# Optimization experiments

Measured on AMD Instinct MI355X. Metric: run time of the kernel, lower is better.

The kernel has to match this reference:

```python
import jax, jax.numpy as jnp
from jax import lax
import numpy as np

B, T, N, C_IN = 32, 24, 2048, 2
HID, EMB, HORIZON, OUT_DIM = 64, 16, 12, 1


def setup_inputs() -> dict:
    key = jax.random.key(0)
    ks = jax.random.split(key, 8)
    s = 0.05
    return {
        "x": jax.random.normal(ks[0], (B, T, N, C_IN), dtype=jnp.float32),
        "E": jax.random.normal(ks[1], (N, EMB), dtype=jnp.float32),
        "W1": jax.random.normal(ks[2], (C_IN + HID, 4 * HID), dtype=jnp.float32) * s,
        "b1": jnp.zeros((4 * HID,), dtype=jnp.float32),
        "W2": jax.random.normal(ks[3], (HID + HID, 4 * HID), dtype=jnp.float32) * s,
        "b2": jnp.zeros((4 * HID,), dtype=jnp.float32),
        "Wp": jax.random.normal(ks[4], (HID, OUT_DIM * HORIZON), dtype=jnp.float32) * s,
        "bp": jnp.zeros((OUT_DIM * HORIZON,), dtype=jnp.float32),
    }


def _cell(A, xt, h, c, W, b):
    # Graph-conv LSTM cell: A @ [x, h] -> 4 gates
    comb = jnp.concatenate([xt, h], axis=-1)            # [B,N,in+H]
    conv = jnp.einsum("nm,bmc->bnc", A, comb)           # adaptive graph conv
    gates = conv @ W + b                                  # [B,N,4H]
    i, f, g, o = jnp.split(gates, 4, axis=-1)
    c_new = jax.nn.sigmoid(f) * c + jax.nn.sigmoid(i) * jnp.tanh(g)
    h_new = jax.nn.sigmoid(o) * jnp.tanh(c_new)
    return h_new, c_new


def reference(x, E, W1, b1, W2, b2, Wp, bp):
    # Adaptive adjacency: softmax(relu(E E^T)) row-normalized
    A = jax.nn.softmax(jax.nn.relu(E @ E.T), axis=1)      # [N,N]
    b, t, n, _ = x.shape
    z = jnp.zeros((b, n, HID), dtype=x.dtype)
    init = ((z, z), (z, z))

    def step(carry, xt):
        (h1, c1), (h2, c2) = carry
        h1, c1 = _cell(A, xt, h1, c1, W1, b1)
        h2, c2 = _cell(A, h1, h2, c2, W2, b2)
        return ((h1, c1), (h2, c2)), None

    carry, _ = lax.scan(step, init, jnp.moveaxis(x, 1, 0))  # scan over T
    h_last = carry[1][0]                                     # [B,N,H]
    out = h_last @ Wp + bp                                   # [B,N,HORIZON*OUT]
    out = out.reshape(b, n, HORIZON, OUT_DIM).transpose(0, 2, 1, 3)
    return out                                               # [B,HORIZON,N,OUT]
```

## Files before the change

### kernel.cpp

```cpp
#include <hip/hip_runtime.h>
#include <hip/hip_bf16.h>
#include <cstddef>
#include <cstdint>

#define NN   2048
#define BB   32
#define TT   24
#define CIN  2
#define HH   64
#define EMBD 16
#define HOR  12
#define XC   (TT*BB*CIN)
#define PW   4096
#define KC   6144
#define NT   96

using bfrag  = __attribute__((ext_vector_type(8))) short;
using f32x4  = __attribute__((ext_vector_type(4))) float;

static __device__ __forceinline__ short f2bf(float f) {
    __hip_bfloat16 h = __float2bfloat16(f);
    return *reinterpret_cast<short*>(&h);
}
static __device__ __forceinline__ float bf2f(short s) {
    __hip_bfloat16 h;
    *reinterpret_cast<short*>(&h) = s;
    return __bfloat162float(h);
}
static __device__ __forceinline__ unsigned int packsplit(float v) {
    short hb = f2bf(v);
    short lb = f2bf(v - bf2f(hb));
    return (unsigned int)(unsigned short)hb | ((unsigned int)(unsigned short)lb << 16);
}
static __device__ __forceinline__ float fsig(float x) {
    return __builtin_amdgcn_rcpf(1.f + __expf(-x));
}
static __device__ __forceinline__ float ftanh(float x) {
    return 1.f - 2.f*__builtin_amdgcn_rcpf(1.f + __expf(2.f*x));
}

#define AS1 __attribute__((address_space(1)))
#define AS3 __attribute__((address_space(3)))
static __device__ __forceinline__ void gload16(const short* g, short* l) {
    __builtin_amdgcn_global_load_lds((const AS1 void*)g, (AS3 void*)l, 16, 0, 0);
}

__global__ __launch_bounds__(256) void compute_A_kernel(const float* __restrict__ E,
                                                        short* __restrict__ A2) {
    __shared__ float srow[NN];
    __shared__ float sred[256];
    int row = blockIdx.x;
    float er[EMBD];
#pragma unroll
    for (int k = 0; k < EMBD; ++k) er[k] = E[row*EMBD + k];
    float lmax = -1e30f;
    for (int j = threadIdx.x; j < NN; j += 256) {
        const float* ej = E + j*EMBD;
        float d = 0.f;
#pragma unroll
        for (int k = 0; k < EMBD; ++k) d = fmaf(er[k], ej[k], d);
        d = fmaxf(d, 0.f);
        srow[j] = d;
        lmax = fmaxf(lmax, d);
    }
    sred[threadIdx.x] = lmax;
    __syncthreads();
    for (int s = 128; s > 0; s >>= 1) {
        if (threadIdx.x < s) sred[threadIdx.x] = fmaxf(sred[threadIdx.x], sred[threadIdx.x+s]);
        __syncthreads();
    }
    float rmax = sred[0];
    __syncthreads();
    float lsum = 0.f;
    for (int j = threadIdx.x; j < NN; j += 256) {
        float e = expf(srow[j] - rmax);
        srow[j] = e;
        lsum += e;
    }
    sred[threadIdx.x] = lsum;
    __syncthreads();
    for (int s = 128; s > 0; s >>= 1) {
        if (threadIdx.x < s) sred[threadIdx.x] += sred[threadIdx.x+s];
        __syncthreads();
    }
    float rinv = 1.f / sred[0];
    for (int j = threadIdx.x; j < NN; j += 256) {
        float v = srow[j] * rinv;
        short h = f2bf(v);
        short l = f2bf(v - bf2f(h));
        size_t base = (size_t)row*KC + j;
        A2[base]        = h;
        A2[base + 2048] = h;
        A2[base + 4096] = l;
    }
}

__global__ void scatter_xall(const float* __restrict__ x,
                             short* __restrict__ hi, short* __restrict__ lo) {
    int idx = blockIdx.x*256 + threadIdx.x;
    int n = idx & (NN-1);
    int col = idx >> 11;
    int c = col & 1, b = (col >> 1) & 31, t = col >> 6;
    float v = x[(size_t)(((size_t)b*TT + t)*NN + n)*CIN + c];
    short h = f2bf(v);
    size_t o = (size_t)col*NN + n;
    hi[o] = h;
    lo[o] = f2bf(v - bf2f(h));
}

__global__ void wsplit_T(const float* __restrict__ W, int rowoff, int Kd,
                         short* __restrict__ hi, short* __restrict__ lo) {
    int id = blockIdx.x*256 + threadIdx.x;
    if (id >= 256*Kd) return;
    int j = id / Kd, c = id - j*Kd;
    float v = W[(size_t)(rowoff + c)*256 + j];
    short h = f2bf(v);
    hi[id] = h;
    lo[id] = f2bf(v - bf2f(h));
}

__global__ __launch_bounds__(256, 3) void gc3_gemm(
        const short* __restrict__ Ahi, const short* __restrict__ Alo,
        const short* __restrict__ Bhi, const short* __restrict__ Blo,
        float* __restrict__ Cout, int outStride, int astr) {
    __shared__ short As[12288];
    short* AsHi = As;
    short* AsLo = As + 2048;
    short* BsHi = As + 4096;
    short* BsLo = As + 8192;
    const int t = threadIdx.x;
    const int w = t >> 6, lane = t & 63;
    const int wm = w >> 1, wn = w & 1;
    const int fr = lane & 15, fc = lane >> 4;
    const int rowbase = blockIdx.y * 64;
    const int colbase = blockIdx.x * 128;

    const int rp = t >> 3, ql = t & 7;
    const int qs = ql ^ (rp & 7);
    const int srow = rp*2 + (qs >> 2);
    const int sch  = (qs & 3) * 8;
    const short* aHiS = Ahi + (size_t)(rowbase + srow)*astr + sch;
    const short* aLoS = Alo + (size_t)(rowbase + srow)*astr + sch;
    const short* bHiS = Bhi + (size_t)(colbase + srow)*NN + sch;
    const short* bLoS = Blo + (size_t)(colbase + srow)*NN + sch;
    const size_t bHalf = (size_t)64*NN;

    short* aHiD  = AsHi + t*8;
    short* aLoD  = AsLo + t*8;
    short* bHiD0 = BsHi + t*8;
    short* bHiD1 = BsHi + 2048 + t*8;
    short* bLoD0 = BsLo + t*8;
    short* bLoD1 = BsLo + 2048 + t*8;

    auto ldsoff = [](int row, int f) {
        int rr = row >> 1;
        int q = (((row & 1) << 2) | f) ^ (rr & 7);
        return rr*64 + q*8;
    };
    int aoff[2], boff[4];
#pragma unroll
    for (int m = 0; m < 2; ++m) aoff[m] = ldsoff(wm*32 + m*16 + fr, fc);
#pragma unroll
    for (int n = 0; n < 4; ++n) boff[n] = ldsoff(wn*64 + n*16 + fr, fc);

    f32x4 acc[2][4];
#pragma unroll
    for (int m = 0; m < 2; ++m)
#pragma unroll
        for (int n = 0; n < 4; ++n)
#pragma unroll
            for (int r = 0; r < 4; ++r) acc[m][n][r] = 0.f;

    for (int k0 = 0; k0 < NN; k0 += 32) {
        gload16(aHiS, aHiD);
        gload16(aLoS, aLoD);
        gload16(bHiS, bHiD0);
        gload16(bHiS + bHalf, bHiD1);
        gload16(bLoS, bLoD0);
        gload16(bLoS + bHalf, bLoD1);
        aHiS += 32; aLoS += 32; bHiS += 32; bLoS += 32;
        __syncthreads();
        bfrag ah[2], al[2], bh[4], bl[4];
#pragma unroll
        for (int m = 0; m < 2; ++m) {
            ah[m] = *(const bfrag*)(AsHi + aoff[m]);
            al[m] = *(const bfrag*)(AsLo + aoff[m]);
        }
#pragma unroll
        for (int n = 0; n < 4; ++n) {
            bh[n] = *(const bfrag*)(BsHi + boff[n]);
            bl[n] = *(const bfrag*)(BsLo + boff[n]);
        }
#pragma unroll
        for (int m = 0; m < 2; ++m)
#pragma unroll
            for (int n = 0; n < 4; ++n) {
                acc[m][n] = __builtin_amdgcn_mfma_f32_16x16x32_bf16(ah[m], bh[n], acc[m][n], 0, 0, 0);
                acc[m][n] = __builtin_amdgcn_mfma_f32_16x16x32_bf16(ah[m], bl[n], acc[m][n], 0, 0, 0);
                acc[m][n] = __builtin_amdgcn_mfma_f32_16x16x32_bf16(al[m], bh[n], acc[m][n], 0, 0, 0);
            }
        __syncthreads();
    }
#pragma unroll
    for (int m = 0; m < 2; ++m) {
        const int gr = rowbase + wm*32 + m*16 + fc*4;
#pragma unroll
        for (int n = 0; n < 4; ++n) {
            const int gc = colbase + wn*64 + n*16 + fr;
#pragma unroll
            for (int r = 0; r < 4; ++r)
                Cout[(size_t)(gr + r)*outStride + gc] = acc[m][n][r];
        }
    }
}

__global__ __launch_bounds__(512, 2) void gemm8p(
        const short* __restrict__ A2, const short* __restrict__ B2,
        unsigned int* __restrict__ Cpk, int colstart) {
    __shared__ short lds[3*24576];
    const int tid = threadIdx.x;
    const int w = tid >> 6, lane = tid & 63;
    const int wm = w >> 2, wn = w & 3;
    const int fr = lane & 15, fc = lane >> 4;
    const int gx = gridDim.x;
    const int nwg = gx * gridDim.y;
    const int fid = blockIdx.y * gx + blockIdx.x;
    const int swz = (fid & 7) * (nwg >> 3) + (fid >> 3);
    const int rowbase = (swz / gx) * 128;
    const int colbase = colstart + (swz % gx) * 256;

    const int srl = tid >> 3;
    const int sck = (tid & 7) ^ (srl & 7);
    const short* aS0 = A2 + (size_t)(rowbase + srl)*KC + sck*8;
    const short* aS1 = A2 + (size_t)(rowbase + 64 + srl)*KC + sck*8;
    const short* bS0 = B2 + (size_t)(colbase + srl)*KC + sck*8;
    const short* bS1 = B2 + (size_t)(colbase + 64 + srl)*KC + sck*8;
    const short* bS2 = B2 + (size_t)(colbase + 128 + srl)*KC + sck*8;
    const short* bS3 = B2 + (size_t)(colbase + 192 + srl)*KC + sck*8;

    auto sw = [](int row, int chunk) {
        int c2 = chunk ^ (row & 7);
        return row*64 + c2*8;
    };
    int aoff[4][2], boff[4][2];
#pragma unroll
    for (int m = 0; m < 4; ++m)
#pragma unroll
        for (int kk = 0; kk < 2; ++kk)
            aoff[m][kk] = sw(wm*64 + m*16 + fr, kk*4 + fc);
#pragma unroll
    for (int n = 0; n < 4; ++n)
#pragma unroll
        for (int kk = 0; kk < 2; ++kk)
            boff[n][kk] = 8192 + sw(wn*64 + n*16 + fr, kk*4 + fc);

    bfrag a[4], b[4];
    f32x4 acc[4][4];
#pragma unroll
    for (int m = 0; m < 4; ++m)
#pragma unroll
        for (int n = 0; n < 4; ++n)
#pragma unroll
            for (int r = 0; r < 4; ++r) acc[m][n][r] = 0.f;

    short* bC = lds;
    short* bN = lds + 24576;
    short* bP = lds + 49152;

    gload16(aS0, bC + tid*8);            gload16(aS1, bC + 4096 + tid*8);
    gload16(bS0, bC + 8192 + tid*8);     gload16(bS1, bC + 12288 + tid*8);
    gload16(bS2, bC + 16384 + tid*8);    gload16(bS3, bC + 20480 + tid*8);
    gload16(aS0 + 64, bN + tid*8);          gload16(aS1 + 64, bN + 4096 + tid*8);
    gload16(bS0 + 64, bN + 8192 + tid*8);   gload16(bS1 + 64, bN + 12288 + tid*8);
    gload16(bS2 + 64, bN + 16384 + tid*8);  gload16(bS3 + 64, bN + 20480 + tid*8);

    for (int t = 0; t < NT; ++t) {
        if (t < NT-1) { asm volatile("s_waitcnt vmcnt(6)" ::: "memory"); }
        else          { asm volatile("s_waitcnt vmcnt(0)" ::: "memory"); }
        __builtin_amdgcn_s_barrier();
        if (t + 2 < NT) {
            const int toff = (t + 2) * 64;
            gload16(aS0 + toff, bP + tid*8);
            gload16(aS1 + toff, bP + 4096 + tid*8);
            gload16(bS0 + toff, bP + 8192 + tid*8);
            gload16(bS1 + toff, bP + 12288 + tid*8);
            gload16(bS2 + toff, bP + 16384 + tid*8);
            gload16(bS3 + toff, bP + 20480 + tid*8);
        }
        __builtin_amdgcn_sched_barrier(0);
#pragma unroll
        for (int kk = 0; kk < 2; ++kk) {
#pragma unroll
            for (int m = 0; m < 4; ++m) a[m] = *(const bfrag*)(bC + aoff[m][kk]);
#pragma unroll
            for (int n = 0; n < 4; ++n) b[n] = *(const bfrag*)(bC + boff[n][kk]);
            __builtin_amdgcn_sched_barrier(0);
            __builtin_amdgcn_s_setprio(1);
#pragma unroll
            for (int m = 0; m < 4; ++m)
#pragma unroll
                for (int n = 0; n < 4; ++n)
                    acc[m][n] = __builtin_amdgcn_mfma_f32_16x16x32_bf16(
                        a[m], b[n], acc[m][n], 0, 0, 0);
            __builtin_amdgcn_s_setprio(0);
            __builtin_amdgcn_sched_barrier(0);
        }
        short* tmp = bC; bC = bN; bN = bP; bP = tmp;
    }
#pragma unroll
    for (int m = 0; m < 4; ++m) {
        const int gr0 = rowbase + wm*64 + m*16 + fc*4;
#pragma unroll
        for (int n = 0; n < 4; ++n) {
            const int gc = colbase + wn*64 + n*16 + fr;
#pragma unroll
            for (int r = 0; r < 4; ++r)
                Cpk[(size_t)(gr0 + r)*PW + gc] = packsplit(acc[m][n][r]);
        }
    }
}

template<int NCH, bool XEP>
static __device__ __forceinline__ void cell_body(
        const unsigned int* __restrict__ P,
        const float* __restrict__ convX,
        const float* __restrict__ Wx,
        const short* __restrict__ Wthi, const short* __restrict__ Wtlo,
        const float* __restrict__ bias,
        float* __restrict__ cbuf,
        short* __restrict__ hout,
        int tstep, int n0blk, int b) {
    const int t = threadIdx.x;
    const int w = t >> 6, lane = t & 63;
    const int fr = lane & 15, fc = lane >> 4;
    constexpr int KW = NCH*32;

    bfrag bh[4][NCH], bl[4][NCH];
#pragma unroll
    for (int g = 0; g < 4; ++g)
#pragma unroll
        for (int ch = 0; ch < NCH; ++ch) {
            size_t o = (size_t)((g*4 + w)*16 + fr)*KW + ch*32 + fc*8;
            bh[g][ch] = *(const bfrag*)(Wthi + o);
            bl[g][ch] = *(const bfrag*)(Wtlo + o);
        }
    const int k = w*16 + fr;
    float bs[4], wx0[4], wx1[4];
#pragma unroll
    for (int g = 0; g < 4; ++g) {
        bs[g] = bias[g*64 + k];
        if (XEP) { wx0[g] = Wx[g*64 + k]; wx1[g] = Wx[256 + g*64 + k]; }
    }
    int colb[NCH];
#pragma unroll
    for (int ch = 0; ch < NCH; ++ch)
        colb[ch] = (NCH == 2 || ch < 2) ? (2048 + b*64 + ch*32)
                                        : (b*64 + (ch-2)*32);
    const int cc = lane >> 4;
    const size_t crow = (size_t)(b*64 + k)*NN;
    const size_t hrow = (size_t)(b*64 + k)*KC;

    for (int nt = 0; nt < 8; ++nt) {
        const int n0 = n0blk + nt*16;
        bfrag ah[NCH], al[NCH];
#pragma unroll
        for (int ch = 0; ch < NCH; ++ch) {
            const unsigned int* ap = P + (size_t)(n0 + fr)*PW + colb[ch] + fc*8;
            uint4 u0 = *(const uint4*)ap;
            uint4 u1 = *(const uint4*)(ap + 4);
            unsigned int uu[8] = {u0.x,u0.y,u0.z,u0.w,u1.x,u1.y,u1.z,u1.w};
#pragma unroll
            for (int i = 0; i < 8; ++i) {
                ah[ch][i] = (short)(uu[i] & 0xffffu);
                al[ch][i] = (short)(uu[i] >> 16);
            }
        }
        f32x4 acc[4];
#pragma unroll
        for (int g = 0; g < 4; ++g)
#pragma unroll
            for (int r = 0; r < 4; ++r) acc[g][r] = 0.f;
#pragma unroll
        for (int ch = 0; ch < NCH; ++ch)
#pragma unroll
            for (int g = 0; g < 4; ++g) {
                acc[g] = __builtin_amdgcn_mfma_f32_16x16x32_bf16(ah[ch], bh[g][ch], acc[g], 0, 0, 0);
                acc[g] = __builtin_amdgcn_mfma_f32_16x16x32_bf16(ah[ch], bl[g][ch], acc[g], 0, 0, 0);
                acc[g] = __builtin_amdgcn_mfma_f32_16x16x32_bf16(al[ch], bh[g][ch], acc[g], 0, 0, 0);
            }
        const int nb = n0 + cc*4;
        float4 cold = *(const float4*)(cbuf + crow + nb);
        float xa0[4], xa1[4];
        if (XEP) {
#pragma unroll
            for (int r = 0; r < 4; ++r) {
                float2 cx = *(const float2*)(convX + (size_t)(nb + r)*XC + tstep*64 + b*2);
                xa0[r] = cx.x; xa1[r] = cx.y;
            }
        }
        float cn[4], hv[4];
#pragma unroll
        for (int r = 0; r < 4; ++r) {
            float pg[4];
#pragma unroll
            for (int g = 0; g < 4; ++g) {
                pg[g] = acc[g][r] + bs[g];
                if (XEP) pg[g] += xa0[r]*wx0[g] + xa1[r]*wx1[g];
            }
            float gi = fsig(pg[0]);
            float gf = fsig(pg[1]);
            float gg = ftanh(pg[2]);
            float go = fsig(pg[3]);
            float co = (&cold.x)[r];
            cn[r] = gf*co + gi*gg;
            hv[r] = go * ftanh(cn[r]);
        }
        *(float4*)(cbuf + crow + nb) = make_float4(cn[0], cn[1], cn[2], cn[3]);
        short hh[4], hl[4];
#pragma unroll
        for (int r = 0; r < 4; ++r) {
            hh[r] = f2bf(hv[r]);
            hl[r] = f2bf(hv[r] - bf2f(hh[r]));
        }
        short4 h4 = make_short4(hh[0], hh[1], hh[2], hh[3]);
        short4 l4 = make_short4(hl[0], hl[1], hl[2], hl[3]);
        *(short4*)(hout + hrow + nb)        = h4;
        *(short4*)(hout + hrow + 2048 + nb) = l4;
        *(short4*)(hout + hrow + 4096 + nb) = h4;
    }
}

template<int NCH, bool XEP>
__global__ __launch_bounds__(256, 2) void cell_mfma(
        const unsigned int* __restrict__ P,
        const float* __restrict__ convX,
        const float* __restrict__ Wx,
        const short* __restrict__ Wthi, const short* __restrict__ Wtlo,
        const float* __restrict__ bias,
        float* __restrict__ cbuf,
        short* __restrict__ hout,
        int tstep) {
    cell_body<NCH, XEP>(P, convX, Wx, Wthi, Wtlo, bias, cbuf, hout,
                        tstep, blockIdx.x*128, blockIdx.y);
}

__global__ __launch_bounds__(256, 2) void cell_fused(
        const unsigned int* __restrict__ P,
        const float* __restrict__ convX,
        const float* __restrict__ Wx1,
        const short* __restrict__ Wt2hi, const short* __restrict__ Wt2lo,
        const short* __restrict__ Wt1hi, const short* __restrict__ Wt1lo,
        const float* __restrict__ b2v, const float* __restrict__ b1v,
        float* __restrict__ cs2, float* __restrict__ cs1,
        short* __restrict__ h2out, short* __restrict__ h1out,
        int tnext) {
    if (blockIdx.z == 0)
        cell_body<4, false>(P, nullptr, nullptr, Wt2hi, Wt2lo, b2v, cs2, h2out,
                            0, blockIdx.x*128, blockIdx.y);
    else
        cell_body<2, true>(P, convX, Wx1, Wt1hi, Wt1lo, b1v, cs1, h1out,
                           tnext, blockIdx.x*128, blockIdx.y);
}

__global__ __launch_bounds__(256) void proj_T(const short* __restrict__ B2,
        const float* __restrict__ Wp, const float* __restrict__ bp,
        float* __restrict__ out) {
    __shared__ float sW[HH*HOR];
    __shared__ float sb[HOR];
    for (int i = threadIdx.x; i < HH*HOR; i += 256) sW[i] = Wp[i];
    if (threadIdx.x < HOR) sb[threadIdx.x] = bp[threadIdx.x];
    __syncthreads();
    int idx = blockIdx.x*256 + threadIdx.x;
    int b = idx >> 11, n = idx & (NN-1);
    float acc[HOR];
#pragma unroll
    for (int j = 0; j < HOR; ++j) acc[j] = sb[j];
    for (int k = 0; k < HH; ++k) {
        size_t row = (size_t)(b*64 + k)*KC + n;
        float h = bf2f(B2[row]) + bf2f(B2[row + 2048]);
#pragma unroll
        for (int j = 0; j < HOR; ++j) acc[j] = fmaf(h, sW[k*HOR + j], acc[j]);
    }
#pragma unroll
    for (int j = 0; j < HOR; ++j)
        out[(size_t)(b*HOR + j)*NN + n] = acc[j];
}

extern "C" void kernel_launch(void* const* d_in, const int* in_sizes, int n_in,
                              void* d_out, int out_size, void* d_ws, size_t ws_size,
                              hipStream_t stream) {
    const float* x  = (const float*)d_in[0];
    const float* E  = (const float*)d_in[1];
    const float* W1 = (const float*)d_in[2];
    const float* b1 = (const float*)d_in[3];
    const float* W2 = (const float*)d_in[4];
    const float* b2 = (const float*)d_in[5];
    const float* Wp = (const float*)d_in[6];
    const float* bp = (const float*)d_in[7];
    float* out = (float*)d_out;

    char* base = (char*)d_ws;
    short* A2     = (short*)base; base += (size_t)NN*KC*2;
    float* convX  = (float*)base; base += (size_t)NN*XC*4;
    unsigned int* P = (unsigned int*)base; base += (size_t)NN*PW*4;
    short* B2     = (short*)base; base += (size_t)PW*KC*2;
    float* cs1    = (float*)base; base += (size_t)NN*NN*4;
    float* cs2    = (float*)base; base += (size_t)NN*NN*4;
    short* Wt2hi  = (short*)base; base += 256*128*2;
    short* Wt2lo  = (short*)base; base += 256*128*2;
    short* Wt1hi  = (short*)base; base += 256*64*2;
    short* Wt1lo  = (short*)base; base += 256*64*2;
    short* XThi = (short*)P;
    short* XTlo = XThi + (size_t)XC*NN;
    short* h2out = B2;
    short* h1out = B2 + (size_t)NN*KC;

    hipMemsetAsync(cs1, 0, (size_t)NN*NN*4, stream);
    hipMemsetAsync(cs2, 0, (size_t)NN*NN*4, stream);

    compute_A_kernel<<<NN, 256, 0, stream>>>(E, A2);
    wsplit_T<<<(256*128 + 255)/256, 256, 0, stream>>>(W2, 0, 128, Wt2hi, Wt2lo);
    wsplit_T<<<(256*64 + 255)/256, 256, 0, stream>>>(W1, 2, 64, Wt1hi, Wt1lo);
    scatter_xall<<<(XC*NN)/256, 256, 0, stream>>>(x, XThi, XTlo);
    gc3_gemm<<<dim3(XC/128, NN/64), 256, 0, stream>>>(
        A2, A2 + 4096, XThi, XTlo, convX, XC, KC);
    hipMemsetAsync(P, 0, (size_t)NN*PW*4, stream);

    cell_mfma<2, true><<<dim3(NN/128, BB), 256, 0, stream>>>(
        P, convX, W1, Wt1hi, Wt1lo, b1, cs1, h1out, 0);
    gemm8p<<<dim3(8, 16), 512, 0, stream>>>(A2, B2, P, 2048);

    for (int t = 0; t < TT; ++t) {
        if (t < TT-1) {
            cell_fused<<<dim3(NN/128, BB, 2), 256, 0, stream>>>(
                P, convX, W1, Wt2hi, Wt2lo, Wt1hi, Wt1lo, b2, b1,
                cs2, cs1, h2out, h1out, t+1);
            gemm8p<<<dim3(16, 16), 512, 0, stream>>>(A2, B2, P, 0);
        } else {
            cell_mfma<4, false><<<dim3(NN/128, BB), 256, 0, stream>>>(
                P, nullptr, nullptr, Wt2hi, Wt2lo, b2, cs2, h2out, 0);
        }
    }
    proj_T<<<(BB*NN)/256, 256, 0, stream>>>(B2, Wp, bp, out);
}
```

Measured before the change: 3.768 ms.

## Store bf16 hi/lo splits separately and issue three 32x32 MFMAs per tile

Replaces the concatenated [hi,hi,lo]×[hi,lo,hi] K=6144 layout with separate hi and lo arrays of K=2048. The per-step graph-conv GEMM now loads each hi fragment once and issues three 32x32x16 MFMAs (hi·hi, hi·lo, lo·hi). This cuts duplicated global and LDS traffic for the hi parts, and the 32x32 MFMA shape is meant to raise MFMA throughput. The cell kernels, the A builder and the projection are updated to write and read the split buffers, and the epilogue maps the 16-value accumulator layout.

```diff
diff --git a/kernel.cpp b/kernel.cpp
--- a/kernel.cpp
+++ b/kernel.cpp
@@ -12,11 +12,12 @@
 #define HOR  12
 #define XC   (TT*BB*CIN)
 #define PW   4096
-#define KC   6144
-#define NT   96
+#define NT2  64
+#define HOFF ((size_t)2048*NN)
 
 using bfrag  = __attribute__((ext_vector_type(8))) short;
 using f32x4  = __attribute__((ext_vector_type(4))) float;
+using f32x16 = __attribute__((ext_vector_type(16))) float;
 
 static __device__ __forceinline__ short f2bf(float f) {
     __hip_bfloat16 h = __float2bfloat16(f);
@@ -46,7 +47,8 @@
 }
 
 __global__ __launch_bounds__(256) void compute_A_kernel(const float* __restrict__ E,
-                                                        short* __restrict__ A2) {
+                                                        short* __restrict__ Ahi,
+                                                        short* __restrict__ Alo) {
     __shared__ float srow[NN];
     __shared__ float sred[256];
     int row = blockIdx.x;
@@ -87,11 +89,8 @@
     for (int j = threadIdx.x; j < NN; j += 256) {
         float v = srow[j] * rinv;
         short h = f2bf(v);
-        short l = f2bf(v - bf2f(h));
-        size_t base = (size_t)row*KC + j;
-        A2[base]        = h;
-        A2[base + 2048] = h;
-        A2[base + 4096] = l;
+        Ahi[(size_t)row*NN + j] = h;
+        Alo[(size_t)row*NN + j] = f2bf(v - bf2f(h));
     }
 }
 
@@ -122,7 +121,7 @@
 __global__ __launch_bounds__(256, 3) void gc3_gemm(
         const short* __restrict__ Ahi, const short* __restrict__ Alo,
         const short* __restrict__ Bhi, const short* __restrict__ Blo,
-        float* __restrict__ Cout, int outStride, int astr) {
+        float* __restrict__ Cout, int outStride) {
     __shared__ short As[12288];
     short* AsHi = As;
     short* AsLo = As + 2048;
@@ -139,8 +138,8 @@
     const int qs = ql ^ (rp & 7);
     const int srow = rp*2 + (qs >> 2);
     const int sch  = (qs & 3) * 8;
-    const short* aHiS = Ahi + (size_t)(rowbase + srow)*astr + sch;
-    const short* aLoS = Alo + (size_t)(rowbase + srow)*astr + sch;
+    const short* aHiS = Ahi + (size_t)(rowbase + srow)*NN + sch;
+    const short* aLoS = Alo + (size_t)(rowbase + srow)*NN + sch;
     const short* bHiS = Bhi + (size_t)(colbase + srow)*NN + sch;
     const short* bLoS = Blo + (size_t)(colbase + srow)*NN + sch;
     const size_t bHalf = (size_t)64*NN;
@@ -214,14 +213,15 @@
     }
 }
 
-__global__ __launch_bounds__(512, 2) void gemm8p(
-        const short* __restrict__ A2, const short* __restrict__ B2,
+__global__ __launch_bounds__(512, 2) void gcsplit(
+        const short* __restrict__ Ahi, const short* __restrict__ Alo,
+        const short* __restrict__ Bhi, const short* __restrict__ Blo,
         unsigned int* __restrict__ Cpk, int colstart) {
     __shared__ short lds[3*24576];
     const int tid = threadIdx.x;
     const int w = tid >> 6, lane = tid & 63;
     const int wm = w >> 2, wn = w & 3;
-    const int fr = lane & 15, fc = lane >> 4;
+    const int lr = lane & 31, lh = lane >> 5;
     const int gx = gridDim.x;
     const int nwg = gx * gridDim.y;
     const int fid = blockIdx.y * gx + blockIdx.x;
@@ -229,93 +229,98 @@
     const int rowbase = (swz / gx) * 128;
     const int colbase = colstart + (swz % gx) * 256;
 
-    const int srl = tid >> 3;
-    const int sck = (tid & 7) ^ (srl & 7);
-    const short* aS0 = A2 + (size_t)(rowbase + srl)*KC + sck*8;
-    const short* aS1 = A2 + (size_t)(rowbase + 64 + srl)*KC + sck*8;
-    const short* bS0 = B2 + (size_t)(colbase + srl)*KC + sck*8;
-    const short* bS1 = B2 + (size_t)(colbase + 64 + srl)*KC + sck*8;
-    const short* bS2 = B2 + (size_t)(colbase + 128 + srl)*KC + sck*8;
-    const short* bS3 = B2 + (size_t)(colbase + 192 + srl)*KC + sck*8;
-
-    auto sw = [](int row, int chunk) {
-        int c2 = chunk ^ (row & 7);
-        return row*64 + c2*8;
+    const int srow = tid >> 2;
+    const int sc   = (tid & 3) ^ ((srow >> 1) & 3);
+    const short* aHiS  = Ahi + (size_t)(rowbase + srow)*NN + sc*8;
+    const short* aLoS  = Alo + (size_t)(rowbase + srow)*NN + sc*8;
+    const short* bHiS0 = Bhi + (size_t)(colbase + srow)*NN + sc*8;
+    const short* bHiS1 = Bhi + (size_t)(colbase + 128 + srow)*NN + sc*8;
+    const short* bLoS0 = Blo + (size_t)(colbase + srow)*NN + sc*8;
+    const short* bLoS1 = Blo + (size_t)(colbase + 128 + srow)*NN + sc*8;
+
+    auto sw2 = [](int row, int c) {
+        return row*32 + (c ^ ((row >> 1) & 3))*8;
     };
-    int aoff[4][2], boff[4][2];
-#pragma unroll
-    for (int m = 0; m < 4; ++m)
-#pragma unroll
-        for (int kk = 0; kk < 2; ++kk)
-            aoff[m][kk] = sw(wm*64 + m*16 + fr, kk*4 + fc);
-#pragma unroll
-    for (int n = 0; n < 4; ++n)
-#pragma unroll
-        for (int kk = 0; kk < 2; ++kk)
-            boff[n][kk] = 8192 + sw(wn*64 + n*16 + fr, kk*4 + fc);
-
-    bfrag a[4], b[4];
-    f32x4 acc[4][4];
-#pragma unroll
-    for (int m = 0; m < 4; ++m)
-#pragma unroll
-        for (int n = 0; n < 4; ++n)
-#pragma unroll
-            for (int r = 0; r < 4; ++r) acc[m][n][r] = 0.f;
+    int aoffH[2][2], boffH[2][2];
+#pragma unroll
+    for (int m = 0; m < 2; ++m)
+#pragma unroll
+        for (int ks = 0; ks < 2; ++ks)
+            aoffH[m][ks] = sw2(wm*64 + m*32 + lr, ks*2 + lh);
+#pragma unroll
+    for (int n = 0; n < 2; ++n)
+#pragma unroll
+        for (int ks = 0; ks < 2; ++ks)
+            boffH[n][ks] = 8192 + sw2(wn*64 + n*32 + lr, ks*2 + lh);
+
+    f32x16 acc[2][2];
+#pragma unroll
+    for (int m = 0; m < 2; ++m)
+#pragma unroll
+        for (int n = 0; n < 2; ++n)
+#pragma unroll
+            for (int r = 0; r < 16; ++r) acc[m][n][r] = 0.f;
 
     short* bC = lds;
     short* bN = lds + 24576;
     short* bP = lds + 49152;
 
-    gload16(aS0, bC + tid*8);            gload16(aS1, bC + 4096 + tid*8);
-    gload16(bS0, bC + 8192 + tid*8);     gload16(bS1, bC + 12288 + tid*8);
-    gload16(bS2, bC + 16384 + tid*8);    gload16(bS3, bC + 20480 + tid*8);
-    gload16(aS0 + 64, bN + tid*8);          gload16(aS1 + 64, bN + 4096 + tid*8);
-    gload16(bS0 + 64, bN + 8192 + tid*8);   gload16(bS1 + 64, bN + 12288 + tid*8);
-    gload16(bS2 + 64, bN + 16384 + tid*8);  gload16(bS3 + 64, bN + 20480 + tid*8);
-
-    for (int t = 0; t < NT; ++t) {
-        if (t < NT-1) { asm volatile("s_waitcnt vmcnt(6)" ::: "memory"); }
-        else          { asm volatile("s_waitcnt vmcnt(0)" ::: "memory"); }
+    auto STAGE = [&](short* dst, int koff) {
+        gload16(aHiS  + koff, dst + tid*8);
+        gload16(aLoS  + koff, dst + 4096  + tid*8);
+        gload16(bHiS0 + koff, dst + 8192  + tid*8);
+        gload16(bHiS1 + koff, dst + 12288 + tid*8);
+        gload16(bLoS0 + koff, dst + 16384 + tid*8);
+        gload16(bLoS1 + koff, dst + 20480 + tid*8);
+    };
+    STAGE(bC, 0);
+    STAGE(bN, 32);
+
+    for (int t = 0; t < NT2; ++t) {
+        if (t < NT2-1) { asm volatile("s_waitcnt vmcnt(6)" ::: "memory"); }
+        else           { asm volatile("s_waitcnt vmcnt(0)" ::: "memory"); }
         __builtin_amdgcn_s_barrier();
-        if (t + 2 < NT) {
-            const int toff = (t + 2) * 64;
-            gload16(aS0 + toff, bP + tid*8);
-            gload16(aS1 + toff, bP + 4096 + tid*8);
-            gload16(bS0 + toff, bP + 8192 + tid*8);
-            gload16(bS1 + toff, bP + 12288 + tid*8);
-            gload16(bS2 + toff, bP + 16384 + tid*8);
-            gload16(bS3 + toff, bP + 20480 + tid*8);
-        }
+        if (t + 2 < NT2) STAGE(bP, (t + 2) * 32);
         __builtin_amdgcn_sched_barrier(0);
 #pragma unroll
-        for (int kk = 0; kk < 2; ++kk) {
-#pragma unroll
-            for (int m = 0; m < 4; ++m) a[m] = *(const bfrag*)(bC + aoff[m][kk]);
-#pragma unroll
-            for (int n = 0; n < 4; ++n) b[n] = *(const bfrag*)(bC + boff[n][kk]);
+        for (int ks = 0; ks < 2; ++ks) {
+            bfrag ah[2], al[2], bh[2], bl[2];
+#pragma unroll
+            for (int m = 0; m < 2; ++m) {
+                ah[m] = *(const bfrag*)(bC + aoffH[m][ks]);
+                al[m] = *(const bfrag*)(bC + 4096 + aoffH[m][ks]);
+            }
+#pragma unroll
+            for (int n = 0; n < 2; ++n) {
+                bh[n] = *(const bfrag*)(bC + boffH[n][ks]);
+                bl[n] = *(const bfrag*)(bC + 8192 + boffH[n][ks]);
+            }
             __builtin_amdgcn_sched_barrier(0);
             __builtin_amdgcn_s_setprio(1);
 #pragma unroll
-            for (int m = 0; m < 4; ++m)
-#pragma unroll
-                for (int n = 0; n < 4; ++n)
-                    acc[m][n] = __builtin_amdgcn_mfma_f32_16x16x32_bf16(
-                        a[m], b[n], acc[m][n], 0, 0, 0);
+            for (int m = 0; m < 2; ++m)
+#pragma unroll
+                for (int n = 0; n < 2; ++n) {
+                    acc[m][n] = __builtin_amdgcn_mfma_f32_32x32x16_bf16(ah[m], bh[n], acc[m][n], 0, 0, 0);
+                    acc[m][n] = __builtin_amdgcn_mfma_f32_32x32x16_bf16(ah[m], bl[n], acc[m][n], 0, 0, 0);
+                    acc[m][n] = __builtin_amdgcn_mfma_f32_32x32x16_bf16(al[m], bh[n], acc[m][n], 0, 0, 0);
+                }
             __builtin_amdgcn_s_setprio(0);
             __builtin_amdgcn_sched_barrier(0);
         }
         short* tmp = bC; bC = bN; bN = bP; bP = tmp;
     }
 #pragma unroll
-    for (int m = 0; m < 4; ++m) {
-        const int gr0 = rowbase + wm*64 + m*16 + fc*4;
-#pragma unroll
-        for (int n = 0; n < 4; ++n) {
-            const int gc = colbase + wn*64 + n*16 + fr;
-#pragma unroll
-            for (int r = 0; r < 4; ++r)
-                Cpk[(size_t)(gr0 + r)*PW + gc] = packsplit(acc[m][n][r]);
+    for (int m = 0; m < 2; ++m) {
+        const int gr0 = rowbase + wm*64 + m*32 + 4*lh;
+#pragma unroll
+        for (int n = 0; n < 2; ++n) {
+            const int gc = colbase + wn*64 + n*32 + lr;
+#pragma unroll
+            for (int r = 0; r < 16; ++r) {
+                int gr = gr0 + (r & 3) + 8*(r >> 2);
+                Cpk[(size_t)gr*PW + gc] = packsplit(acc[m][n][r]);
+            }
         }
     }
 }
@@ -328,21 +333,21 @@
         const short* __restrict__ Wthi, const short* __restrict__ Wtlo,
         const float* __restrict__ bias,
         float* __restrict__ cbuf,
-        short* __restrict__ hout,
+        short* __restrict__ bhi, short* __restrict__ blo,
         int tstep, int n0blk, int b) {
     const int t = threadIdx.x;
     const int w = t >> 6, lane = t & 63;
     const int fr = lane & 15, fc = lane >> 4;
     constexpr int KW = NCH*32;
 
-    bfrag bh[4][NCH], bl[4][NCH];
+    bfrag bhw[4][NCH], blw[4][NCH];
 #pragma unroll
     for (int g = 0; g < 4; ++g)
 #pragma unroll
         for (int ch = 0; ch < NCH; ++ch) {
             size_t o = (size_t)((g*4 + w)*16 + fr)*KW + ch*32 + fc*8;
-            bh[g][ch] = *(const bfrag*)(Wthi + o);
-            bl[g][ch] = *(const bfrag*)(Wtlo + o);
+            bhw[g][ch] = *(const bfrag*)(Wthi + o);
+            blw[g][ch] = *(const bfrag*)(Wtlo + o);
         }
     const int k = w*16 + fr;
     float bs[4], wx0[4], wx1[4];
@@ -358,7 +363,6 @@
                                         : (b*64 + (ch-2)*32);
     const int cc = lane >> 4;
     const size_t crow = (size_t)(b*64 + k)*NN;
-    const size_t hrow = (size_t)(b*64 + k)*KC;
 
     for (int nt = 0; nt < 8; ++nt) {
         const int n0 = n0blk + nt*16;
@@ -384,9 +388,9 @@
         for (int ch = 0; ch < NCH; ++ch)
 #pragma unroll
             for (int g = 0; g < 4; ++g) {
-                acc[g] = __builtin_amdgcn_mfma_f32_16x16x32_bf16(ah[ch], bh[g][ch], acc[g], 0, 0, 0);
-                acc[g] = __builtin_amdgcn_mfma_f32_16x16x32_bf16(ah[ch], bl[g][ch], acc[g], 0, 0, 0);
-                acc[g] = __builtin_amdgcn_mfma_f32_16x16x32_bf16(al[ch], bh[g][ch], acc[g], 0, 0, 0);
+                acc[g] = __builtin_amdgcn_mfma_f32_16x16x32_bf16(ah[ch], bhw[g][ch], acc[g], 0, 0, 0);
+                acc[g] = __builtin_amdgcn_mfma_f32_16x16x32_bf16(ah[ch], blw[g][ch], acc[g], 0, 0, 0);
+                acc[g] = __builtin_amdgcn_mfma_f32_16x16x32_bf16(al[ch], bhw[g][ch], acc[g], 0, 0, 0);
             }
         const int nb = n0 + cc*4;
         float4 cold = *(const float4*)(cbuf + crow + nb);
@@ -422,11 +426,8 @@
             hh[r] = f2bf(hv[r]);
             hl[r] = f2bf(hv[r] - bf2f(hh[r]));
         }
-        short4 h4 = make_short4(hh[0], hh[1], hh[2], hh[3]);
-        short4 l4 = make_short4(hl[0], hl[1], hl[2], hl[3]);
-        *(short4*)(hout + hrow + nb)        = h4;
-        *(short4*)(hout + hrow + 2048 + nb) = l4;
-        *(short4*)(hout + hrow + 4096 + nb) = h4;
+        *(short4*)(bhi + crow + nb) = make_short4(hh[0], hh[1], hh[2], hh[3]);
+        *(short4*)(blo + crow + nb) = make_short4(hl[0], hl[1], hl[2], hl[3]);
     }
 }
 
@@ -438,9 +439,9 @@
         const short* __restrict__ Wthi, const short* __restrict__ Wtlo,
         const float* __restrict__ bias,
         float* __restrict__ cbuf,
-        short* __restrict__ hout,
+        short* __restrict__ bhi, short* __restrict__ blo,
         int tstep) {
-    cell_body<NCH, XEP>(P, convX, Wx, Wthi, Wtlo, bias, cbuf, hout,
+    cell_body<NCH, XEP>(P, convX, Wx, Wthi, Wtlo, bias, cbuf, bhi, blo,
                         tstep, blockIdx.x*128, blockIdx.y);
 }
 
@@ -452,19 +453,19 @@
         const short* __restrict__ Wt1hi, const short* __restrict__ Wt1lo,
         const float* __restrict__ b2v, const float* __restrict__ b1v,
         float* __restrict__ cs2, float* __restrict__ cs1,
-        short* __restrict__ h2out, short* __restrict__ h1out,
+        short* __restrict__ Bhi, short* __restrict__ Blo,
         int tnext) {
     if (blockIdx.z == 0)
-        cell_body<4, false>(P, nullptr, nullptr, Wt2hi, Wt2lo, b2v, cs2, h2out,
-                            0, blockIdx.x*128, blockIdx.y);
+        cell_body<4, false>(P, nullptr, nullptr, Wt2hi, Wt2lo, b2v, cs2,
+                            Bhi, Blo, 0, blockIdx.x*128, blockIdx.y);
     else
-        cell_body<2, true>(P, convX, Wx1, Wt1hi, Wt1lo, b1v, cs1, h1out,
-                           tnext, blockIdx.x*128, blockIdx.y);
-}
-
-__global__ __launch_bounds__(256) void proj_T(const short* __restrict__ B2,
-        const float* __restrict__ Wp, const float* __restrict__ bp,
-        float* __restrict__ out) {
+        cell_body<2, true>(P, convX, Wx1, Wt1hi, Wt1lo, b1v, cs1,
+                           Bhi + HOFF, Blo + HOFF, tnext, blockIdx.x*128, blockIdx.y);
+}
+
+__global__ __launch_bounds__(256) void proj_T(const short* __restrict__ Bhi,
+        const short* __restrict__ Blo, const float* __restrict__ Wp,
+        const float* __restrict__ bp, float* __restrict__ out) {
     __shared__ float sW[HH*HOR];
     __shared__ float sb[HOR];
     for (int i = threadIdx.x; i < HH*HOR; i += 256) sW[i] = Wp[i];
@@ -476,8 +477,8 @@
 #pragma unroll
     for (int j = 0; j < HOR; ++j) acc[j] = sb[j];
     for (int k = 0; k < HH; ++k) {
-        size_t row = (size_t)(b*64 + k)*KC + n;
-        float h = bf2f(B2[row]) + bf2f(B2[row + 2048]);
+        size_t row = (size_t)(b*64 + k)*NN + n;
+        float h = bf2f(Bhi[row]) + bf2f(Blo[row]);
 #pragma unroll
         for (int j = 0; j < HOR; ++j) acc[j] = fmaf(h, sW[k*HOR + j], acc[j]);
     }
@@ -500,10 +501,12 @@
     float* out = (float*)d_out;
 
     char* base = (char*)d_ws;
-    short* A2     = (short*)base; base += (size_t)NN*KC*2;
+    short* Ahi    = (short*)base; base += (size_t)NN*NN*2;
+    short* Alo    = (short*)base; base += (size_t)NN*NN*2;
     float* convX  = (float*)base; base += (size_t)NN*XC*4;
     unsigned int* P = (unsigned int*)base; base += (size_t)NN*PW*4;
-    short* B2     = (short*)base; base += (size_t)PW*KC*2;
+    short* Bhi    = (short*)base; base += (size_t)2*NN*NN*2;
+    short* Blo    = (short*)base; base += (size_t)2*NN*NN*2;
     float* cs1    = (float*)base; base += (size_t)NN*NN*4;
     float* cs2    = (float*)base; base += (size_t)NN*NN*4;
     short* Wt2hi  = (short*)base; base += 256*128*2;
@@ -512,34 +515,32 @@
     short* Wt1lo  = (short*)base; base += 256*64*2;
     short* XThi = (short*)P;
     short* XTlo = XThi + (size_t)XC*NN;
-    short* h2out = B2;
-    short* h1out = B2 + (size_t)NN*KC;
 
     hipMemsetAsync(cs1, 0, (size_t)NN*NN*4, stream);
     hipMemsetAsync(cs2, 0, (size_t)NN*NN*4, stream);
 
-    compute_A_kernel<<<NN, 256, 0, stream>>>(E, A2);
+    compute_A_kernel<<<NN, 256, 0, stream>>>(E, Ahi, Alo);
     wsplit_T<<<(256*128 + 255)/256, 256, 0, stream>>>(W2, 0, 128, Wt2hi, Wt2lo);
     wsplit_T<<<(256*64 + 255)/256, 256, 0, stream>>>(W1, 2, 64, Wt1hi, Wt1lo);
     scatter_xall<<<(XC*NN)/256, 256, 0, stream>>>(x, XThi, XTlo);
     gc3_gemm<<<dim3(XC/128, NN/64), 256, 0, stream>>>(
-        A2, A2 + 4096, XThi, XTlo, convX, XC, KC);
+        Ahi, Alo, XThi, XTlo, convX, XC);
     hipMemsetAsync(P, 0, (size_t)NN*PW*4, stream);
 
     cell_mfma<2, true><<<dim3(NN/128, BB), 256, 0, stream>>>(
-        P, convX, W1, Wt1hi, Wt1lo, b1, cs1, h1out, 0);
-    gemm8p<<<dim3(8, 16), 512, 0, stream>>>(A2, B2, P, 2048);
+        P, convX, W1, Wt1hi, Wt1lo, b1, cs1, Bhi + HOFF, Blo + HOFF, 0);
+    gcsplit<<<dim3(8, 16), 512, 0, stream>>>(Ahi, Alo, Bhi, Blo, P, 2048);
 
     for (int t = 0; t < TT; ++t) {
         if (t < TT-1) {
             cell_fused<<<dim3(NN/128, BB, 2), 256, 0, stream>>>(
                 P, convX, W1, Wt2hi, Wt2lo, Wt1hi, Wt1lo, b2, b1,
-                cs2, cs1, h2out, h1out, t+1);
-            gemm8p<<<dim3(16, 16), 512, 0, stream>>>(A2, B2, P, 0);
+                cs2, cs1, Bhi, Blo, t+1);
+            gcsplit<<<dim3(16, 16), 512, 0, stream>>>(Ahi, Alo, Bhi, Blo, P, 0);
         } else {
             cell_mfma<4, false><<<dim3(NN/128, BB), 256, 0, stream>>>(
-                P, nullptr, nullptr, Wt2hi, Wt2lo, b2, cs2, h2out, 0);
-        }
-    }
-    proj_T<<<(BB*NN)/256, 256, 0, stream>>>(B2, Wp, bp, out);
-}
+                P, nullptr, nullptr, Wt2hi, Wt2lo, b2, cs2, Bhi, Blo, 0);
+        }
+    }
+    proj_T<<<(BB*NN)/256, 256, 0, stream>>>(Bhi, Blo, Wp, bp, out);
+}
```

After: 3.717 ms. No clear change (-1.3%).
